# Kernel tuning notes

Measured on AMD Instinct MI355X. Metric: run time of the kernel, lower is better.

Reference implementation:

```python
import jax, jax.numpy as jnp
import numpy as np

DIM = 128
POS_HID = 64
ATTN_HID = DIM * 4
K_NEIGH = 16


def _mlp2(x, w1, b1, w2, b2):
    # Linear -> ReLU -> Linear (weights stored as (in, out))
    return jax.nn.relu(x @ w1 + b1) @ w2 + b2


def setup_inputs() -> dict:
    key = jax.random.key(0)
    ks = jax.random.split(key, 12)
    B, N = 2, 512
    s = 0.05
    return {
        "x": jax.random.normal(ks[0], (B, DIM, N), jnp.float32),
        "pos": jax.random.normal(ks[1], (B, N, 3), jnp.float32),
        "w_qkv": jax.random.normal(ks[2], (DIM, 3 * DIM), jnp.float32) * s,
        "pos_w1": jax.random.normal(ks[3], (3, POS_HID), jnp.float32) * s,
        "pos_b1": jnp.zeros((POS_HID,), jnp.float32),
        "pos_w2": jax.random.normal(ks[4], (POS_HID, DIM), jnp.float32) * s,
        "pos_b2": jnp.zeros((DIM,), jnp.float32),
        "attn_w1": jax.random.normal(ks[5], (DIM, ATTN_HID), jnp.float32) * s,
        "attn_b1": jnp.zeros((ATTN_HID,), jnp.float32),
        "attn_w2": jax.random.normal(ks[6], (ATTN_HID, DIM), jnp.float32) * s,
        "attn_b2": jnp.zeros((DIM,), jnp.float32),
    }


def reference(x, pos, w_qkv, pos_w1, pos_b1, pos_w2, pos_b2,
              attn_w1, attn_b1, attn_w2, attn_b2):
    # x: (B, dim, N) -> (B, N, dim)
    xt = jnp.swapaxes(x, 1, 2)
    B, N, d = xt.shape

    qkv = xt @ w_qkv                           # (B, N, 3d), no bias
    q, k, v = jnp.split(qkv, 3, axis=-1)

    rel_pos = pos[:, :, None, :] - pos[:, None, :, :]          # (B, N, N, 3)
    rel_pos_emb = _mlp2(rel_pos, pos_w1, pos_b1, pos_w2, pos_b2)  # (B, N, N, d)
    qk_rel = q[:, :, None, :] - k[:, None, :, :]               # (B, N, N, d)

    # KNN: smallest euclidean rel distances per query point
    rel_dist = jnp.sqrt(jnp.sum(rel_pos * rel_pos, axis=-1))   # (B, N, N)
    _, idx = jax.lax.top_k(-rel_dist, K_NEIGH)                 # (B, N, K)

    idxe = idx[..., None]                                      # (B, N, K, 1)
    v_g = v[jnp.arange(B)[:, None, None], idx]                 # (B, N, K, d)
    qk_g = jnp.take_along_axis(qk_rel, idxe, axis=2)           # (B, N, K, d)
    pe_g = jnp.take_along_axis(rel_pos_emb, idxe, axis=2)      # (B, N, K, d)

    v_g = v_g + pe_g
    sim = _mlp2(qk_g + pe_g, attn_w1, attn_b1, attn_w2, attn_b2)  # (B, N, K, d)
    attn = jax.nn.softmax(sim, axis=-2)                        # softmax over neighbors
    agg = jnp.einsum('bikd,bikd->bid', attn, v_g)              # (B, N, d)
    return jnp.swapaxes(agg, 1, 2)                             # (B, d, N)
```

## Files before the change

kernel.cpp:

```cpp
#include <hip/hip_runtime.h>
#include <math.h>

#define DIM 128
#define N_PTS 512
#define K_NEIGH 16
#define POS_HID 64
#define ATTN_HID 512

typedef __attribute__((ext_vector_type(8))) short short8;
typedef __attribute__((ext_vector_type(4))) float f32x4;
typedef unsigned short us;
typedef unsigned long long ull;

__device__ __forceinline__ us f2b(float f) {
    unsigned int u = __builtin_bit_cast(unsigned int, f);
    u += 0x7fffu + ((u >> 16) & 1u);
    return (us)(u >> 16);
}

__device__ __forceinline__ ull shflx64(ull v, int m) {
    int lo = __shfl_xor((int)(unsigned int)v, m);
    int hi = __shfl_xor((int)(unsigned int)(v >> 32), m);
    return ((ull)(unsigned int)hi << 32) | (unsigned int)lo;
}

__global__ void pack_kernel(const float* __restrict__ wqkv,
                            const float* __restrict__ aw1,
                            const float* __restrict__ aw2,
                            const float* __restrict__ pw2,
                            us* __restrict__ p0, us* __restrict__ p1,
                            us* __restrict__ p2, us* __restrict__ p3) {
    int t = blockIdx.x * 256 + threadIdx.x;
    if (t < 49152) {
        int j = t & 7, l = (t >> 3) & 63, rem = t >> 9;
        int nt = rem % 24, ks = rem / 24;
        int k = ks * 32 + (l >> 4) * 8 + j, n = nt * 16 + (l & 15);
        p0[t] = f2b(wqkv[k * 384 + n]);
    } else if (t < 114688) {
        int u = t - 49152;
        int j = u & 7, l = (u >> 3) & 63, nt = (u >> 9) & 31, ks = u >> 14;
        int k = ks * 32 + (l >> 4) * 8 + j, n = nt * 16 + (l & 15);
        p1[u] = f2b(aw1[k * ATTN_HID + n]);
    } else if (t < 180224) {
        int u = t - 114688;
        int j = u & 7, l = (u >> 3) & 63, nt = (u >> 9) & 7, ch = u >> 12;
        int k = ch * 32 + (l >> 4) * 8 + j, n = nt * 16 + (l & 15);
        p2[u] = f2b(aw2[k * DIM + n]);
    } else if (t < 188416) {
        int u = t - 180224;
        int j = u & 7, l = (u >> 3) & 63, nt = (u >> 9) & 7, ks = u >> 12;
        int k = ks * 32 + (l >> 4) * 8 + j, n = nt * 16 + (l & 15);
        p3[u] = f2b(pw2[k * DIM + n]);
    }
}

__global__ __launch_bounds__(512)
void qkv_mfma_kernel(const float* __restrict__ x,
                     const us* __restrict__ p0,
                     float* __restrict__ qkv) {
    __shared__ __align__(16) us xA[16][136];
    const int tid = threadIdx.x;
    const int w = tid >> 6, lane = tid & 63, quad = lane >> 4, lq = lane & 15;
    const int n0 = blockIdx.x * 16;
    const int b = n0 >> 9, nn = n0 & (N_PTS - 1);
#pragma unroll
    for (int rr = 0; rr < 4; ++rr) {
        int id = rr * 512 + tid;
        int d = id >> 4, i = id & 15;
        xA[i][d] = f2b(x[(size_t)(b * DIM + d) * N_PTS + nn + i]);
    }
    __syncthreads();
    short8 a[4];
#pragma unroll
    for (int ks = 0; ks < 4; ++ks)
        a[ks] = *(const short8*)&xA[lq][ks * 32 + quad * 8];
#pragma unroll
    for (int i = 0; i < 3; ++i) {
        int nt = w * 3 + i;
        f32x4 acc = {0.f, 0.f, 0.f, 0.f};
#pragma unroll
        for (int ks = 0; ks < 4; ++ks) {
            const short8 bf = *(const short8*)(p0 + (size_t)((ks * 24 + nt) * 64 + lane) * 8);
            acc = __builtin_amdgcn_mfma_f32_16x16x32_bf16(a[ks], bf, acc, 0, 0, 0);
        }
#pragma unroll
        for (int r = 0; r < 4; ++r)
            qkv[(size_t)(n0 + quad * 4 + r) * 384 + nt * 16 + lq] = acc[r];
    }
}

__global__ __launch_bounds__(256)
void attn_fused_kernel(const float* __restrict__ pos,
                       const float* __restrict__ qkv,
                       const float* __restrict__ pw1,
                       const float* __restrict__ pb1,
                       const float* __restrict__ pb2,
                       const us* __restrict__ p1,
                       const us* __restrict__ p2,
                       const us* __restrict__ p3,
                       const float* __restrict__ ab1,
                       float* __restrict__ out) {
    __shared__ __align__(16) us hinA[4][16][136];
    __shared__ __align__(16) us h1s[4][16][40];
    __shared__ int nbrs[4][16];

    const int tid = threadIdx.x;
    const int w = tid >> 6, lane = tid & 63, quad = lane >> 4, lq = lane & 15;
    const int g = blockIdx.x * 4 + w, b = g >> 9, n = g & (N_PTS - 1);

    short8 b3f[2][8];
#pragma unroll
    for (int ks = 0; ks < 2; ++ks)
#pragma unroll
        for (int nt = 0; nt < 8; ++nt)
            b3f[ks][nt] = *(const short8*)(p3 + (size_t)((ks * 8 + nt) * 64 + lane) * 8);

    float w1x[2][8], w1y[2][8], w1z[2][8], w1b[2][8];
#pragma unroll
    for (int ks = 0; ks < 2; ++ks)
#pragma unroll
        for (int jj = 0; jj < 8; ++jj) {
            int c = ks * 32 + quad * 8 + jj;
            w1x[ks][jj] = pw1[c];
            w1y[ks][jj] = pw1[64 + c];
            w1z[ks][jj] = pw1[128 + c];
            w1b[ks][jj] = pb1[c];
        }

    float qvr[8], pb2r[8];
#pragma unroll
    for (int nt = 0; nt < 8; ++nt) {
        qvr[nt]  = qkv[(size_t)g * 384 + nt * 16 + lq];
        pb2r[nt] = pb2[nt * 16 + lq];
    }

    {
        const float pix = pos[g * 3 + 0], piy = pos[g * 3 + 1], piz = pos[g * 3 + 2];
        float d2[8];
#pragma unroll
        for (int rr = 0; rr < 8; ++rr) {
            int j = rr * 64 + lane;
            float dx = pix - pos[(b * N_PTS + j) * 3 + 0];
            float dy = piy - pos[(b * N_PTS + j) * 3 + 1];
            float dz = piz - pos[(b * N_PTS + j) * 3 + 2];
            d2[rr] = dx * dx + dy * dy + dz * dz;
        }
        for (int r = 0; r < K_NEIGH; ++r) {
            ull key = ~0ULL;
#pragma unroll
            for (int rr = 0; rr < 8; ++rr) {
                unsigned int fb = __builtin_bit_cast(unsigned int, d2[rr]);
                ull k2 = ((ull)fb << 32) | (unsigned int)(rr * 64 + lane);
                key = k2 < key ? k2 : key;
            }
#pragma unroll
            for (int off = 32; off > 0; off >>= 1) {
                ull o = shflx64(key, off);
                key = o < key ? o : key;
            }
            unsigned int jw = (unsigned int)key;
            if (lane == 0) nbrs[w][r] = (int)jw;
            if (lane == (int)(jw & 63)) d2[jw >> 6] = __builtin_inff();
        }
    }

    short8 pha[2];
    {
        const int jn = nbrs[w][lq];
        float rx = pos[g * 3 + 0] - pos[(b * N_PTS + jn) * 3 + 0];
        float ry = pos[g * 3 + 1] - pos[(b * N_PTS + jn) * 3 + 1];
        float rz = pos[g * 3 + 2] - pos[(b * N_PTS + jn) * 3 + 2];
#pragma unroll
        for (int ks = 0; ks < 2; ++ks) {
            short8 f;
#pragma unroll
            for (int jj = 0; jj < 8; ++jj) {
                float h = rx * w1x[ks][jj] + ry * w1y[ks][jj] + rz * w1z[ks][jj] + w1b[ks][jj];
                f[jj] = (short)f2b(fmaxf(h, 0.f));
            }
            pha[ks] = f;
        }
    }

    f32x4 pe[8];
#pragma unroll
    for (int nt = 0; nt < 8; ++nt) {
        f32x4 acc = {0.f, 0.f, 0.f, 0.f};
        acc = __builtin_amdgcn_mfma_f32_16x16x32_bf16(pha[0], b3f[0][nt], acc, 0, 0, 0);
        acc = __builtin_amdgcn_mfma_f32_16x16x32_bf16(pha[1], b3f[1][nt], acc, 0, 0, 0);
#pragma unroll
        for (int r = 0; r < 4; ++r) pe[nt][r] = acc[r] + pb2r[nt];
    }

    f32x4 vg[8];
    {
        int jr[4];
#pragma unroll
        for (int r = 0; r < 4; ++r) jr[r] = nbrs[w][quad * 4 + r];
#pragma unroll
        for (int nt = 0; nt < 8; ++nt) {
            int d = nt * 16 + lq;
#pragma unroll
            for (int r = 0; r < 4; ++r) {
                const float* kv = qkv + (size_t)(b * N_PTS + jr[r]) * 384;
                float pp = pe[nt][r];
                hinA[w][quad * 4 + r][d] = f2b(qvr[nt] - kv[128 + d] + pp);
                vg[nt][r] = kv[256 + d] + pp;
            }
        }
    }

    short8 a1f[4];
#pragma unroll
    for (int ks = 0; ks < 4; ++ks)
        a1f[ks] = *(const short8*)&hinA[w][lq][ks * 32 + quad * 8];

    f32x4 c2[8];
#pragma unroll
    for (int nt = 0; nt < 8; ++nt) c2[nt] = (f32x4){0.f, 0.f, 0.f, 0.f};

    short8 p1f[2][2][4];
    short8 p2f[2][8];
#pragma unroll
    for (int t = 0; t < 2; ++t)
#pragma unroll
        for (int ks = 0; ks < 4; ++ks)
            p1f[0][t][ks] = *(const short8*)(p1 + (size_t)(((ks << 5) + t) * 64 + lane) * 8);
#pragma unroll
    for (int nt2 = 0; nt2 < 8; ++nt2)
        p2f[0][nt2] = *(const short8*)(p2 + (size_t)(nt2 * 64 + lane) * 8);

#pragma unroll
    for (int ch = 0; ch < 16; ++ch) {
        const int cur = ch & 1, nxt = cur ^ 1;
        if (ch < 15) {
#pragma unroll
            for (int t = 0; t < 2; ++t)
#pragma unroll
                for (int ks = 0; ks < 4; ++ks)
                    p1f[nxt][t][ks] = *(const short8*)(p1 + (size_t)(((ks << 5) + (ch + 1) * 2 + t) * 64 + lane) * 8);
        }
#pragma unroll
        for (int t = 0; t < 2; ++t) {
            int nt = ch * 2 + t;
            f32x4 acc = {0.f, 0.f, 0.f, 0.f};
#pragma unroll
            for (int ks = 0; ks < 4; ++ks)
                acc = __builtin_amdgcn_mfma_f32_16x16x32_bf16(a1f[ks], p1f[cur][t][ks], acc, 0, 0, 0);
            float bias = ab1[nt * 16 + lq];
#pragma unroll
            for (int r = 0; r < 4; ++r)
                h1s[w][quad * 4 + r][t * 16 + lq] = f2b(fmaxf(acc[r] + bias, 0.f));
        }
        if (ch < 15) {
#pragma unroll
            for (int nt2 = 0; nt2 < 8; ++nt2)
                p2f[nxt][nt2] = *(const short8*)(p2 + (size_t)((((ch + 1) << 3) + nt2) * 64 + lane) * 8);
        }
        const short8 a2 = *(const short8*)&h1s[w][lq][quad * 8];
#pragma unroll
        for (int nt2 = 0; nt2 < 8; ++nt2)
            c2[nt2] = __builtin_amdgcn_mfma_f32_16x16x32_bf16(a2, p2f[cur][nt2], c2[nt2], 0, 0, 0);
    }

#pragma unroll
    for (int nt2 = 0; nt2 < 8; ++nt2) {
        f32x4 s4 = c2[nt2];
        float m = fmaxf(fmaxf(s4[0], s4[1]), fmaxf(s4[2], s4[3]));
        m = fmaxf(m, __shfl_xor(m, 16));
        m = fmaxf(m, __shfl_xor(m, 32));
        float e0 = __expf(s4[0] - m), e1 = __expf(s4[1] - m);
        float e2 = __expf(s4[2] - m), e3 = __expf(s4[3] - m);
        float s = e0 + e1 + e2 + e3;
        f32x4 v4 = vg[nt2];
        float a = e0 * v4[0] + e1 * v4[1] + e2 * v4[2] + e3 * v4[3];
        s += __shfl_xor(s, 16); s += __shfl_xor(s, 32);
        a += __shfl_xor(a, 16); a += __shfl_xor(a, 32);
        if (quad == 0)
            out[(size_t)(b * DIM + nt2 * 16 + lq) * N_PTS + n] = a / s;
    }
}

extern "C" void kernel_launch(void* const* d_in, const int* in_sizes, int n_in,
                              void* d_out, int out_size, void* d_ws, size_t ws_size,
                              hipStream_t stream) {
    const float* x    = (const float*)d_in[0];
    const float* pos  = (const float*)d_in[1];
    const float* wqkv = (const float*)d_in[2];
    const float* pw1  = (const float*)d_in[3];
    const float* pb1  = (const float*)d_in[4];
    const float* pw2  = (const float*)d_in[5];
    const float* pb2  = (const float*)d_in[6];
    const float* aw1  = (const float*)d_in[7];
    const float* ab1  = (const float*)d_in[8];
    const float* aw2  = (const float*)d_in[9];
    float* out = (float*)d_out;

    int B = in_sizes[0] / (DIM * N_PTS);
    int npts = B * N_PTS;

    char* ws = (char*)d_ws;
    float* qkv = (float*)ws;
    us* p0 = (us*)(ws + (size_t)npts * 384 * 4);
    us* p1 = p0 + 49152;
    us* p2 = p1 + 65536;
    us* p3 = p2 + 65536;

    pack_kernel<<<736, 256, 0, stream>>>(wqkv, aw1, aw2, pw2, p0, p1, p2, p3);
    qkv_mfma_kernel<<<npts / 16, 512, 0, stream>>>(x, p0, qkv);
    attn_fused_kernel<<<npts / 4, 256, 0, stream>>>(pos, qkv,
                                                    pw1, pb1, pb2,
                                                    p1, p2, p3, ab1, out);
}
```

Baseline: 100.8 us.

## Split attention MLP hidden dimension across two waves per query point

Each block now handles one query point with two waves instead of four points with one wave each. Each wave redundantly runs KNN and the position embedding, then computes half of the 512-wide hidden layer. Partial second-layer results are combined through shared memory before the softmax and aggregation. Weights are reloaded rather than held in registers to cut register pressure and raise occupancy, at the cost of duplicated KNN and positional work per point plus a block barrier.

```diff
diff --git a/kernel.cpp b/kernel.cpp
--- a/kernel.cpp
+++ b/kernel.cpp
@@ -89,7 +89,7 @@
     }
 }
 
-__global__ __launch_bounds__(256)
+__global__ __launch_bounds__(128, 2)
 void attn_fused_kernel(const float* __restrict__ pos,
                        const float* __restrict__ qkv,
                        const float* __restrict__ pw1,
@@ -100,32 +100,14 @@
                        const us* __restrict__ p3,
                        const float* __restrict__ ab1,
                        float* __restrict__ out) {
-    __shared__ __align__(16) us hinA[4][16][136];
-    __shared__ __align__(16) us h1s[4][16][40];
-    __shared__ int nbrs[4][16];
+    __shared__ __align__(16) us hinA[2][16][136];
+    __shared__ __align__(16) us h1s[2][16][40];
+    __shared__ float c2s[32][66];
+    __shared__ int nbrs[2][16];
 
     const int tid = threadIdx.x;
-    const int w = tid >> 6, lane = tid & 63, quad = lane >> 4, lq = lane & 15;
-    const int g = blockIdx.x * 4 + w, b = g >> 9, n = g & (N_PTS - 1);
-
-    short8 b3f[2][8];
-#pragma unroll
-    for (int ks = 0; ks < 2; ++ks)
-#pragma unroll
-        for (int nt = 0; nt < 8; ++nt)
-            b3f[ks][nt] = *(const short8*)(p3 + (size_t)((ks * 8 + nt) * 64 + lane) * 8);
-
-    float w1x[2][8], w1y[2][8], w1z[2][8], w1b[2][8];
-#pragma unroll
-    for (int ks = 0; ks < 2; ++ks)
-#pragma unroll
-        for (int jj = 0; jj < 8; ++jj) {
-            int c = ks * 32 + quad * 8 + jj;
-            w1x[ks][jj] = pw1[c];
-            w1y[ks][jj] = pw1[64 + c];
-            w1z[ks][jj] = pw1[128 + c];
-            w1b[ks][jj] = pb1[c];
-        }
+    const int s = tid >> 6, lane = tid & 63, quad = lane >> 4, lq = lane & 15;
+    const int g = blockIdx.x, b = g >> 9, n = g & (N_PTS - 1);
 
     float qvr[8], pb2r[8];
 #pragma unroll
@@ -159,14 +141,14 @@
                 key = o < key ? o : key;
             }
             unsigned int jw = (unsigned int)key;
-            if (lane == 0) nbrs[w][r] = (int)jw;
+            if (lane == 0) nbrs[s][r] = (int)jw;
             if (lane == (int)(jw & 63)) d2[jw >> 6] = __builtin_inff();
         }
     }
 
     short8 pha[2];
     {
-        const int jn = nbrs[w][lq];
+        const int jn = nbrs[s][lq];
         float rx = pos[g * 3 + 0] - pos[(b * N_PTS + jn) * 3 + 0];
         float ry = pos[g * 3 + 1] - pos[(b * N_PTS + jn) * 3 + 1];
         float rz = pos[g * 3 + 2] - pos[(b * N_PTS + jn) * 3 + 2];
@@ -175,7 +157,8 @@
             short8 f;
 #pragma unroll
             for (int jj = 0; jj < 8; ++jj) {
-                float h = rx * w1x[ks][jj] + ry * w1y[ks][jj] + rz * w1z[ks][jj] + w1b[ks][jj];
+                int c = ks * 32 + quad * 8 + jj;
+                float h = rx * pw1[c] + ry * pw1[64 + c] + rz * pw1[128 + c] + pb1[c];
                 f[jj] = (short)f2b(fmaxf(h, 0.f));
             }
             pha[ks] = f;
@@ -185,55 +168,54 @@
     f32x4 pe[8];
 #pragma unroll
     for (int nt = 0; nt < 8; ++nt) {
+        const short8 b0 = *(const short8*)(p3 + (size_t)((0 * 8 + nt) * 64 + lane) * 8);
+        const short8 b1 = *(const short8*)(p3 + (size_t)((1 * 8 + nt) * 64 + lane) * 8);
         f32x4 acc = {0.f, 0.f, 0.f, 0.f};
-        acc = __builtin_amdgcn_mfma_f32_16x16x32_bf16(pha[0], b3f[0][nt], acc, 0, 0, 0);
-        acc = __builtin_amdgcn_mfma_f32_16x16x32_bf16(pha[1], b3f[1][nt], acc, 0, 0, 0);
+        acc = __builtin_amdgcn_mfma_f32_16x16x32_bf16(pha[0], b0, acc, 0, 0, 0);
+        acc = __builtin_amdgcn_mfma_f32_16x16x32_bf16(pha[1], b1, acc, 0, 0, 0);
 #pragma unroll
         for (int r = 0; r < 4; ++r) pe[nt][r] = acc[r] + pb2r[nt];
     }
 
-    f32x4 vg[8];
-    {
-        int jr[4];
-#pragma unroll
-        for (int r = 0; r < 4; ++r) jr[r] = nbrs[w][quad * 4 + r];
-#pragma unroll
-        for (int nt = 0; nt < 8; ++nt) {
-            int d = nt * 16 + lq;
-#pragma unroll
-            for (int r = 0; r < 4; ++r) {
-                const float* kv = qkv + (size_t)(b * N_PTS + jr[r]) * 384;
-                float pp = pe[nt][r];
-                hinA[w][quad * 4 + r][d] = f2b(qvr[nt] - kv[128 + d] + pp);
-                vg[nt][r] = kv[256 + d] + pp;
-            }
+    int jr[4];
+#pragma unroll
+    for (int r = 0; r < 4; ++r) jr[r] = nbrs[s][quad * 4 + r];
+#pragma unroll
+    for (int nt = 0; nt < 8; ++nt) {
+        int d = nt * 16 + lq;
+#pragma unroll
+        for (int r = 0; r < 4; ++r) {
+            const float* kv = qkv + (size_t)(b * N_PTS + jr[r]) * 384;
+            hinA[s][quad * 4 + r][d] = f2b(qvr[nt] - kv[128 + d] + pe[nt][r]);
         }
     }
 
     short8 a1f[4];
 #pragma unroll
     for (int ks = 0; ks < 4; ++ks)
-        a1f[ks] = *(const short8*)&hinA[w][lq][ks * 32 + quad * 8];
+        a1f[ks] = *(const short8*)&hinA[s][lq][ks * 32 + quad * 8];
 
     f32x4 c2[8];
 #pragma unroll
     for (int nt = 0; nt < 8; ++nt) c2[nt] = (f32x4){0.f, 0.f, 0.f, 0.f};
 
+    const int ch0 = s * 8;
     short8 p1f[2][2][4];
     short8 p2f[2][8];
 #pragma unroll
     for (int t = 0; t < 2; ++t)
 #pragma unroll
         for (int ks = 0; ks < 4; ++ks)
-            p1f[0][t][ks] = *(const short8*)(p1 + (size_t)(((ks << 5) + t) * 64 + lane) * 8);
+            p1f[0][t][ks] = *(const short8*)(p1 + (size_t)(((ks << 5) + ch0 * 2 + t) * 64 + lane) * 8);
 #pragma unroll
     for (int nt2 = 0; nt2 < 8; ++nt2)
-        p2f[0][nt2] = *(const short8*)(p2 + (size_t)(nt2 * 64 + lane) * 8);
-
-#pragma unroll
-    for (int ch = 0; ch < 16; ++ch) {
-        const int cur = ch & 1, nxt = cur ^ 1;
-        if (ch < 15) {
+        p2f[0][nt2] = *(const short8*)(p2 + (size_t)((ch0 * 8 + nt2) * 64 + lane) * 8);
+
+#pragma unroll
+    for (int cc = 0; cc < 8; ++cc) {
+        const int ch = ch0 + cc;
+        const int cur = cc & 1, nxt = cur ^ 1;
+        if (cc < 7) {
 #pragma unroll
             for (int t = 0; t < 2; ++t)
 #pragma unroll
@@ -250,34 +232,54 @@
             float bias = ab1[nt * 16 + lq];
 #pragma unroll
             for (int r = 0; r < 4; ++r)
-                h1s[w][quad * 4 + r][t * 16 + lq] = f2b(fmaxf(acc[r] + bias, 0.f));
-        }
-        if (ch < 15) {
+                h1s[s][quad * 4 + r][t * 16 + lq] = f2b(fmaxf(acc[r] + bias, 0.f));
+        }
+        if (cc < 7) {
 #pragma unroll
             for (int nt2 = 0; nt2 < 8; ++nt2)
                 p2f[nxt][nt2] = *(const short8*)(p2 + (size_t)((((ch + 1) << 3) + nt2) * 64 + lane) * 8);
         }
-        const short8 a2 = *(const short8*)&h1s[w][lq][quad * 8];
+        const short8 a2 = *(const short8*)&h1s[s][lq][quad * 8];
 #pragma unroll
         for (int nt2 = 0; nt2 < 8; ++nt2)
             c2[nt2] = __builtin_amdgcn_mfma_f32_16x16x32_bf16(a2, p2f[cur][nt2], c2[nt2], 0, 0, 0);
     }
 
-#pragma unroll
-    for (int nt2 = 0; nt2 < 8; ++nt2) {
-        f32x4 s4 = c2[nt2];
-        float m = fmaxf(fmaxf(s4[0], s4[1]), fmaxf(s4[2], s4[3]));
-        m = fmaxf(m, __shfl_xor(m, 16));
-        m = fmaxf(m, __shfl_xor(m, 32));
-        float e0 = __expf(s4[0] - m), e1 = __expf(s4[1] - m);
-        float e2 = __expf(s4[2] - m), e3 = __expf(s4[3] - m);
-        float s = e0 + e1 + e2 + e3;
-        f32x4 v4 = vg[nt2];
-        float a = e0 * v4[0] + e1 * v4[1] + e2 * v4[2] + e3 * v4[3];
-        s += __shfl_xor(s, 16); s += __shfl_xor(s, 32);
-        a += __shfl_xor(a, 16); a += __shfl_xor(a, 32);
-        if (quad == 0)
-            out[(size_t)(b * DIM + nt2 * 16 + lq) * N_PTS + n] = a / s;
+    if (s == 0) {
+#pragma unroll
+        for (int nt2 = 0; nt2 < 8; ++nt2)
+#pragma unroll
+            for (int r = 0; r < 4; ++r)
+                c2s[nt2 * 4 + r][lane] = c2[nt2][r];
+    }
+    __syncthreads();
+    if (s == 1) {
+        f32x4 vg[8];
+#pragma unroll
+        for (int nt2 = 0; nt2 < 8; ++nt2) {
+            int d = nt2 * 16 + lq;
+#pragma unroll
+            for (int r = 0; r < 4; ++r)
+                vg[nt2][r] = qkv[(size_t)(b * N_PTS + jr[r]) * 384 + 256 + d] + pe[nt2][r];
+        }
+#pragma unroll
+        for (int nt2 = 0; nt2 < 8; ++nt2) {
+            f32x4 s4;
+#pragma unroll
+            for (int r = 0; r < 4; ++r) s4[r] = c2[nt2][r] + c2s[nt2 * 4 + r][lane];
+            float m = fmaxf(fmaxf(s4[0], s4[1]), fmaxf(s4[2], s4[3]));
+            m = fmaxf(m, __shfl_xor(m, 16));
+            m = fmaxf(m, __shfl_xor(m, 32));
+            float e0 = __expf(s4[0] - m), e1 = __expf(s4[1] - m);
+            float e2 = __expf(s4[2] - m), e3 = __expf(s4[3] - m);
+            float ss = e0 + e1 + e2 + e3;
+            f32x4 v4 = vg[nt2];
+            float a = e0 * v4[0] + e1 * v4[1] + e2 * v4[2] + e3 * v4[3];
+            ss += __shfl_xor(ss, 16); ss += __shfl_xor(ss, 32);
+            a  += __shfl_xor(a, 16);  a  += __shfl_xor(a, 32);
+            if (quad == 0)
+                out[(size_t)(b * DIM + nt2 * 16 + lq) * N_PTS + n] = a / ss;
+        }
     }
 }
 
@@ -308,7 +310,7 @@
 
     pack_kernel<<<736, 256, 0, stream>>>(wqkv, aw1, aw2, pw2, p0, p1, p2, p3);
     qkv_mfma_kernel<<<npts / 16, 512, 0, stream>>>(x, p0, qkv);
-    attn_fused_kernel<<<npts / 4, 256, 0, stream>>>(pos, qkv,
-                                                    pw1, pb1, pb2,
-                                                    p1, p2, p3, ab1, out);
-}
+    attn_fused_kernel<<<npts, 128, 0, stream>>>(pos, qkv,
+                                                pw1, pb1, pb2,
+                                                p1, p2, p3, ab1, out);
+}
```

New measurement: 103.1 us. 2.3% more time.
